# Kernel tuning notes

Measured on AMD Instinct MI355X. Metric: run time of the kernel, lower is better.

The kernel has to match this reference:

```python
import jax, jax.numpy as jnp
import numpy as np

HIDDEN = 768  # hidden_dim of the embedding matrix
VOCAB = 30522


def setup_inputs() -> dict:
    key = jax.random.key(0)
    k1, k2, k3, k4, k5, k6 = jax.random.split(key, 6)
    core = jax.random.normal(k1, (40, 256, 256), dtype=jnp.float32)
    f0 = jax.random.normal(k2, (40, 40), dtype=jnp.float32)
    f1 = jax.random.normal(k3, (768, 256), dtype=jnp.float32)
    f2 = jax.random.normal(k4, (768, 256), dtype=jnp.float32)
    ids = jax.random.randint(k5, (8192,), 0, VOCAB, dtype=jnp.int32)
    x = jax.random.normal(k6, (8192, 768), dtype=jnp.float32)  # unused by forward, kept for signature parity
    return {"x": x, "ids": ids, "core": core, "f0": f0, "f1": f1, "f2": f2}


def reference(x, ids, core, f0, f1, f2):
    # tucker_to_tensor: core x_0 f0 x_1 f1 x_2 f2 -> (40, 768, 768)
    res = jnp.einsum('abc,ia,jb,kc->ijk', core, f0, f1, f2)
    # flatten to padded embedding table (30720, 768) and gather requested rows
    table = res.reshape(-1, HIDDEN)
    return table[ids, :]
```

## Files before the change

### kernel.cpp

```cpp
#include <hip/hip_runtime.h>


#define A_DIM 40
#define BC 65536
#define C_DIM 256
#define HID 768

typedef __attribute__((ext_vector_type(8))) short short8;
typedef __attribute__((ext_vector_type(4))) float floatx4;

#define AS1 __attribute__((address_space(1)))
#define AS3 __attribute__((address_space(3)))

__device__ __forceinline__ void gl2lds16(const unsigned short* g, unsigned short* l) {
    __builtin_amdgcn_global_load_lds((const AS1 unsigned int*)g, (AS3 unsigned int*)l,
                                     16, 0, 0);
}

__device__ __forceinline__ unsigned short f2bf(float f) {
    unsigned int u = __builtin_bit_cast(unsigned int, f);
    u += 0x7FFFu + ((u >> 16) & 1u);
    return (unsigned short)(u >> 16);
}

__global__ __launch_bounds__(256) void k01_fused(const float* __restrict__ core,
                                                 const float* __restrict__ f0,
                                                 const float* __restrict__ f1,
                                                 const float* __restrict__ f2,
                                                 unsigned short* __restrict__ A1t,
                                                 unsigned short* __restrict__ f1b,
                                                 unsigned short* __restrict__ f2b) {
    const int bid = blockIdx.x;
    const int tid = threadIdx.x;
    if (bid < 512) {
        __shared__ float f0s[200];
        __shared__ unsigned short tt[32 * 34];
        const int i0 = (bid >> 6) * 5;
        const int tile = bid & 63;
        const int b0 = (tile >> 3) * 32;
        const int c0 = (tile & 7) * 32;
        if (tid < 200) f0s[tid] = f0[i0 * A_DIM + tid];
        __syncthreads();

        const int pb = (tid >> 4) * 2;
        const int pc = (tid & 15) * 2;
        float acc[5][4];
#pragma unroll
        for (int ii = 0; ii < 5; ++ii)
#pragma unroll
            for (int e = 0; e < 4; ++e) acc[ii][e] = 0.f;

        const float* cp0 = core + (b0 + pb) * 256 + (c0 + pc);
        for (int a = 0; a < A_DIM; ++a) {
            const float* cp = cp0 + a * BC;
            const float2 r0 = *(const float2*)cp;
            const float2 r1 = *(const float2*)(cp + 256);
#pragma unroll
            for (int ii = 0; ii < 5; ++ii) {
                const float fa = f0s[ii * A_DIM + a];
                acc[ii][0] += fa * r0.x;
                acc[ii][1] += fa * r0.y;
                acc[ii][2] += fa * r1.x;
                acc[ii][3] += fa * r1.y;
            }
        }
        const int rc = tid >> 3;
        const int rb4 = (tid & 7) * 4;
#pragma unroll
        for (int ii = 0; ii < 5; ++ii) {
            if (ii) __syncthreads();
            unsigned short e00 = f2bf(acc[ii][0]);
            unsigned short e10 = f2bf(acc[ii][2]);
            unsigned short e01 = f2bf(acc[ii][1]);
            unsigned short e11 = f2bf(acc[ii][3]);
            *(unsigned int*)&tt[pc * 34 + pb]       = (unsigned int)e00 | ((unsigned int)e10 << 16);
            *(unsigned int*)&tt[(pc + 1) * 34 + pb] = (unsigned int)e01 | ((unsigned int)e11 << 16);
            __syncthreads();
            unsigned short o[4];
#pragma unroll
            for (int u = 0; u < 4; ++u) o[u] = tt[rc * 34 + rb4 + u];
            unsigned int lo = (unsigned int)o[0] | ((unsigned int)o[1] << 16);
            unsigned int hi = (unsigned int)o[2] | ((unsigned int)o[3] << 16);
            *(uint2*)&A1t[(size_t)(i0 + ii) * BC + (c0 + rc) * 256 + b0 + rb4] = make_uint2(lo, hi);
        }
    } else {
        const int idx = (bid - 512) * 256 + tid;
        const float* src;
        unsigned short* dst;
        int off;
        if (idx < 49152) { src = f1; dst = f1b; off = idx; }
        else             { src = f2; dst = f2b; off = idx - 49152; }
        const float4 v = *(const float4*)&src[off * 4];
        const unsigned int lo = (unsigned int)f2bf(v.x) | ((unsigned int)f2bf(v.y) << 16);
        const unsigned int hi = (unsigned int)f2bf(v.z) | ((unsigned int)f2bf(v.w) << 16);
        *(uint2*)&dst[off * 4] = make_uint2(lo, hi);
    }
}

__global__ __launch_bounds__(256) void k2_gemm(const unsigned short* __restrict__ f1b,
                                               const unsigned short* __restrict__ A1t,
                                               unsigned short* __restrict__ A2) {
    const int i  = blockIdx.z;
    const int j0 = blockIdx.x * 64;
    const int c0 = blockIdx.y * 64;
    const unsigned short* __restrict__ Bsrc = A1t + i * BC;

    __shared__ unsigned short As[64 * 32];
    __shared__ unsigned short Bs[64 * 32];

    const int tid = threadIdx.x;
    const int lane = tid & 63, wave = tid >> 6;
    const int wm = (wave >> 1) * 32, wn = (wave & 1) * 32;
    const int l16 = lane & 15, q = lane >> 4;

    const int r0 = tid >> 2, o0 = (tid & 3) * 8;
    unsigned short* AsW = &As[wave * 512];
    unsigned short* BsW = &Bs[wave * 512];

    floatx4 acc[2][2];
#pragma unroll
    for (int p = 0; p < 2; ++p)
#pragma unroll
        for (int r = 0; r < 2; ++r) acc[p][r] = (floatx4)0.f;

    for (int kk = 0; kk < C_DIM; kk += 32) {
        gl2lds16(&f1b[(j0 + r0) * 256 + kk + o0], AsW);
        gl2lds16(&Bsrc[(c0 + r0) * 256 + kk + o0], BsW);
        __syncthreads();
        short8 af[2], bf[2];
#pragma unroll
        for (int p = 0; p < 2; ++p) af[p] = *(const short8*)&As[(wm + p * 16 + l16) * 32 + q * 8];
#pragma unroll
        for (int r = 0; r < 2; ++r) bf[r] = *(const short8*)&Bs[(wn + r * 16 + l16) * 32 + q * 8];
#pragma unroll
        for (int p = 0; p < 2; ++p)
#pragma unroll
            for (int r = 0; r < 2; ++r)
                acc[p][r] = __builtin_amdgcn_mfma_f32_16x16x32_bf16(af[p], bf[r], acc[p][r], 0, 0, 0);
        __syncthreads();
    }
    unsigned short* __restrict__ Cout = A2 + (size_t)i * HID * C_DIM;
#pragma unroll
    for (int p = 0; p < 2; ++p)
#pragma unroll
        for (int r = 0; r < 2; ++r)
#pragma unroll
            for (int rr = 0; rr < 4; ++rr) {
                const int row = j0 + wm + p * 16 + q * 4 + rr;
                const int col = c0 + wn + r * 16 + l16;
                Cout[row * 256 + col] = f2bf(acc[p][r][rr]);
            }
}

__global__ __launch_bounds__(256) void k3_gemm(const unsigned short* __restrict__ A2,
                                               const unsigned short* __restrict__ f2b,
                                               const int* __restrict__ ids,
                                               float* __restrict__ out) {
    const int n0 = blockIdx.x * 64;
    const int k0 = blockIdx.y * 64;

    __shared__ int ids_s[64];
    __shared__ unsigned short As[64 * 32];
    __shared__ unsigned short Bs[64 * 32];

    const int tid = threadIdx.x;
    if (tid < 64) ids_s[tid] = ids[n0 + tid];
    __syncthreads();

    const int lane = tid & 63, wave = tid >> 6;
    const int wm = (wave >> 1) * 32, wn = (wave & 1) * 32;
    const int l16 = lane & 15, q = lane >> 4;

    const int r0 = tid >> 2, o0 = (tid & 3) * 8;
    const size_t ga = (size_t)ids_s[r0] * 256;
    unsigned short* AsW = &As[wave * 512];
    unsigned short* BsW = &Bs[wave * 512];

    floatx4 acc[2][2];
#pragma unroll
    for (int p = 0; p < 2; ++p)
#pragma unroll
        for (int r = 0; r < 2; ++r) acc[p][r] = (floatx4)0.f;

    for (int kk = 0; kk < C_DIM; kk += 32) {
        gl2lds16(&A2[ga + kk + o0], AsW);
        gl2lds16(&f2b[(k0 + r0) * 256 + kk + o0], BsW);
        __syncthreads();
        short8 af[2], bf[2];
#pragma unroll
        for (int p = 0; p < 2; ++p) af[p] = *(const short8*)&As[(wm + p * 16 + l16) * 32 + q * 8];
#pragma unroll
        for (int r = 0; r < 2; ++r) bf[r] = *(const short8*)&Bs[(wn + r * 16 + l16) * 32 + q * 8];
#pragma unroll
        for (int p = 0; p < 2; ++p)
#pragma unroll
            for (int r = 0; r < 2; ++r)
                acc[p][r] = __builtin_amdgcn_mfma_f32_16x16x32_bf16(af[p], bf[r], acc[p][r], 0, 0, 0);
        __syncthreads();
    }
#pragma unroll
    for (int p = 0; p < 2; ++p)
#pragma unroll
        for (int r = 0; r < 2; ++r)
#pragma unroll
            for (int rr = 0; rr < 4; ++rr) {
                const int row = n0 + wm + p * 16 + q * 4 + rr;
                const int col = k0 + wn + r * 16 + l16;
                out[(size_t)row * HID + col] = acc[p][r][rr];
            }
}

extern "C" void kernel_launch(void* const* d_in, const int* in_sizes, int n_in,
                              void* d_out, int out_size, void* d_ws, size_t ws_size,
                              hipStream_t stream) {
    const int*   ids  = (const int*)d_in[1];
    const float* core = (const float*)d_in[2];
    const float* f0   = (const float*)d_in[3];
    const float* f1   = (const float*)d_in[4];
    const float* f2   = (const float*)d_in[5];
    float* out = (float*)d_out;

    char* ws = (char*)d_ws;
    unsigned short* A1t = (unsigned short*)ws;
    unsigned short* A2  = (unsigned short*)(ws + 5242880);
    unsigned short* f1b = (unsigned short*)(ws + 20971520);
    unsigned short* f2b = (unsigned short*)(ws + 21364736);

    k01_fused<<<896, 256, 0, stream>>>(core, f0, f1, f2, A1t, f1b, f2b);
    k2_gemm<<<dim3(12, 4, A_DIM), 256, 0, stream>>>(f1b, A1t, A2);
    k3_gemm<<<dim3(128, 12), 256, 0, stream>>>(A2, f2b, ids, out);
}
```

Before: 114.4 us.

## Enlarge GEMM tiles to 128x128 and merge batch axis in k2

Both GEMM kernels move from 64x64 to 128x128 output tiles, with each wave computing a 64x64 sub-tile (4x4 MFMA fragments) and each thread issuing two LDS async loads per operand per k-step. k2 also folds the 40-way batch dimension into the column axis, treating A1t as one 10240x256 matrix and scattering results back into the per-slice A2 layout. The goal is more MFMA work per LDS load and barrier and fewer blocks. The cost is more accumulator registers per thread and much fewer blocks: 480 for k2 and 384 for k3, which may underfill the GPU's compute units.

```diff
diff --git a/kernel.cpp b/kernel.cpp
--- a/kernel.cpp
+++ b/kernel.cpp
@@ -100,108 +100,110 @@
 __global__ __launch_bounds__(256) void k2_gemm(const unsigned short* __restrict__ f1b,
                                                const unsigned short* __restrict__ A1t,
                                                unsigned short* __restrict__ A2) {
-    const int i  = blockIdx.z;
-    const int j0 = blockIdx.x * 64;
-    const int c0 = blockIdx.y * 64;
-    const unsigned short* __restrict__ Bsrc = A1t + i * BC;
-
-    __shared__ unsigned short As[64 * 32];
-    __shared__ unsigned short Bs[64 * 32];
+    const int j0  = blockIdx.x * 128;
+    const int cb0 = blockIdx.y * 128;
+
+    __shared__ unsigned short As[128 * 32];
+    __shared__ unsigned short Bs[128 * 32];
 
     const int tid = threadIdx.x;
     const int lane = tid & 63, wave = tid >> 6;
-    const int wm = (wave >> 1) * 32, wn = (wave & 1) * 32;
+    const int wm = (wave >> 1) * 64, wn = (wave & 1) * 64;
     const int l16 = lane & 15, q = lane >> 4;
 
-    const int r0 = tid >> 2, o0 = (tid & 3) * 8;
-    unsigned short* AsW = &As[wave * 512];
-    unsigned short* BsW = &Bs[wave * 512];
-
-    floatx4 acc[2][2];
-#pragma unroll
-    for (int p = 0; p < 2; ++p)
-#pragma unroll
-        for (int r = 0; r < 2; ++r) acc[p][r] = (floatx4)0.f;
+    floatx4 acc[4][4];
+#pragma unroll
+    for (int p = 0; p < 4; ++p)
+#pragma unroll
+        for (int r = 0; r < 4; ++r) acc[p][r] = (floatx4)0.f;
 
     for (int kk = 0; kk < C_DIM; kk += 32) {
-        gl2lds16(&f1b[(j0 + r0) * 256 + kk + o0], AsW);
-        gl2lds16(&Bsrc[(c0 + r0) * 256 + kk + o0], BsW);
-        __syncthreads();
-        short8 af[2], bf[2];
-#pragma unroll
-        for (int p = 0; p < 2; ++p) af[p] = *(const short8*)&As[(wm + p * 16 + l16) * 32 + q * 8];
-#pragma unroll
-        for (int r = 0; r < 2; ++r) bf[r] = *(const short8*)&Bs[(wn + r * 16 + l16) * 32 + q * 8];
-#pragma unroll
-        for (int p = 0; p < 2; ++p)
-#pragma unroll
-            for (int r = 0; r < 2; ++r)
+#pragma unroll
+        for (int u = 0; u < 2; ++u) {
+            const int chunk = (wave * 2 + u) * 64 + lane;
+            const int row = chunk >> 2;
+            const int sl  = (chunk & 3) * 8;
+            gl2lds16(&f1b[(j0 + row) * 256 + kk + sl],                 &As[(wave * 2 + u) * 512]);
+            gl2lds16(&A1t[(size_t)(cb0 + row) * 256 + kk + sl],        &Bs[(wave * 2 + u) * 512]);
+        }
+        __syncthreads();
+        short8 af[4], bf[4];
+#pragma unroll
+        for (int p = 0; p < 4; ++p) af[p] = *(const short8*)&As[(wm + p * 16 + l16) * 32 + q * 8];
+#pragma unroll
+        for (int r = 0; r < 4; ++r) bf[r] = *(const short8*)&Bs[(wn + r * 16 + l16) * 32 + q * 8];
+#pragma unroll
+        for (int p = 0; p < 4; ++p)
+#pragma unroll
+            for (int r = 0; r < 4; ++r)
                 acc[p][r] = __builtin_amdgcn_mfma_f32_16x16x32_bf16(af[p], bf[r], acc[p][r], 0, 0, 0);
         __syncthreads();
     }
-    unsigned short* __restrict__ Cout = A2 + (size_t)i * HID * C_DIM;
-#pragma unroll
-    for (int p = 0; p < 2; ++p)
-#pragma unroll
-        for (int r = 0; r < 2; ++r)
+#pragma unroll
+    for (int p = 0; p < 4; ++p)
+#pragma unroll
+        for (int r = 0; r < 4; ++r) {
+            const int col = cb0 + wn + r * 16 + l16;
+            const size_t base = (size_t)(col >> 8) * (768 * 256) + (size_t)(col & 255);
 #pragma unroll
             for (int rr = 0; rr < 4; ++rr) {
                 const int row = j0 + wm + p * 16 + q * 4 + rr;
-                const int col = c0 + wn + r * 16 + l16;
-                Cout[row * 256 + col] = f2bf(acc[p][r][rr]);
+                A2[base + (size_t)row * 256] = f2bf(acc[p][r][rr]);
             }
+        }
 }
 
 __global__ __launch_bounds__(256) void k3_gemm(const unsigned short* __restrict__ A2,
                                                const unsigned short* __restrict__ f2b,
                                                const int* __restrict__ ids,
                                                float* __restrict__ out) {
-    const int n0 = blockIdx.x * 64;
-    const int k0 = blockIdx.y * 64;
-
-    __shared__ int ids_s[64];
-    __shared__ unsigned short As[64 * 32];
-    __shared__ unsigned short Bs[64 * 32];
+    const int n0 = blockIdx.x * 128;
+    const int k0 = blockIdx.y * 128;
+
+    __shared__ int ids_s[128];
+    __shared__ unsigned short As[128 * 32];
+    __shared__ unsigned short Bs[128 * 32];
 
     const int tid = threadIdx.x;
-    if (tid < 64) ids_s[tid] = ids[n0 + tid];
+    if (tid < 128) ids_s[tid] = ids[n0 + tid];
     __syncthreads();
 
     const int lane = tid & 63, wave = tid >> 6;
-    const int wm = (wave >> 1) * 32, wn = (wave & 1) * 32;
+    const int wm = (wave >> 1) * 64, wn = (wave & 1) * 64;
     const int l16 = lane & 15, q = lane >> 4;
 
-    const int r0 = tid >> 2, o0 = (tid & 3) * 8;
-    const size_t ga = (size_t)ids_s[r0] * 256;
-    unsigned short* AsW = &As[wave * 512];
-    unsigned short* BsW = &Bs[wave * 512];
-
-    floatx4 acc[2][2];
-#pragma unroll
-    for (int p = 0; p < 2; ++p)
-#pragma unroll
-        for (int r = 0; r < 2; ++r) acc[p][r] = (floatx4)0.f;
+    floatx4 acc[4][4];
+#pragma unroll
+    for (int p = 0; p < 4; ++p)
+#pragma unroll
+        for (int r = 0; r < 4; ++r) acc[p][r] = (floatx4)0.f;
 
     for (int kk = 0; kk < C_DIM; kk += 32) {
-        gl2lds16(&A2[ga + kk + o0], AsW);
-        gl2lds16(&f2b[(k0 + r0) * 256 + kk + o0], BsW);
-        __syncthreads();
-        short8 af[2], bf[2];
-#pragma unroll
-        for (int p = 0; p < 2; ++p) af[p] = *(const short8*)&As[(wm + p * 16 + l16) * 32 + q * 8];
-#pragma unroll
-        for (int r = 0; r < 2; ++r) bf[r] = *(const short8*)&Bs[(wn + r * 16 + l16) * 32 + q * 8];
-#pragma unroll
-        for (int p = 0; p < 2; ++p)
-#pragma unroll
-            for (int r = 0; r < 2; ++r)
+#pragma unroll
+        for (int u = 0; u < 2; ++u) {
+            const int chunk = (wave * 2 + u) * 64 + lane;
+            const int row = chunk >> 2;
+            const int sl  = (chunk & 3) * 8;
+            gl2lds16(&A2[(size_t)ids_s[row] * 256 + kk + sl],   &As[(wave * 2 + u) * 512]);
+            gl2lds16(&f2b[(k0 + row) * 256 + kk + sl],          &Bs[(wave * 2 + u) * 512]);
+        }
+        __syncthreads();
+        short8 af[4], bf[4];
+#pragma unroll
+        for (int p = 0; p < 4; ++p) af[p] = *(const short8*)&As[(wm + p * 16 + l16) * 32 + q * 8];
+#pragma unroll
+        for (int r = 0; r < 4; ++r) bf[r] = *(const short8*)&Bs[(wn + r * 16 + l16) * 32 + q * 8];
+#pragma unroll
+        for (int p = 0; p < 4; ++p)
+#pragma unroll
+            for (int r = 0; r < 4; ++r)
                 acc[p][r] = __builtin_amdgcn_mfma_f32_16x16x32_bf16(af[p], bf[r], acc[p][r], 0, 0, 0);
         __syncthreads();
     }
 #pragma unroll
-    for (int p = 0; p < 2; ++p)
-#pragma unroll
-        for (int r = 0; r < 2; ++r)
+    for (int p = 0; p < 4; ++p)
+#pragma unroll
+        for (int r = 0; r < 4; ++r)
 #pragma unroll
             for (int rr = 0; rr < 4; ++rr) {
                 const int row = n0 + wm + p * 16 + q * 4 + rr;
@@ -227,6 +229,6 @@
     unsigned short* f2b = (unsigned short*)(ws + 21364736);
 
     k01_fused<<<896, 256, 0, stream>>>(core, f0, f1, f2, A1t, f1b, f2b);
-    k2_gemm<<<dim3(12, 4, A_DIM), 256, 0, stream>>>(f1b, A1t, A2);
-    k3_gemm<<<dim3(128, 12), 256, 0, stream>>>(A2, f2b, ids, out);
-}
+    k2_gemm<<<dim3(6, 80), 256, 0, stream>>>(f1b, A1t, A2);
+    k3_gemm<<<dim3(64, 6), 256, 0, stream>>>(A2, f2b, ids, out);
+}
```

After: 112.0 us. 1.02x faster.
